# Kernel tuning notes

Measured on AMD Instinct MI355X. Metric: run time of the kernel, lower is better.

## Reference

```python
import jax, jax.numpy as jnp
import numpy as np
from jax import lax

VOCAB, EMB, H, L, B = 32000, 512, 512, 256, 64


def _flip_bwd(t):
    # t: (L, B, 2, ...); reverse time for the backward direction (dir index 1)
    return jnp.stack([t[:, :, 0], t[::-1, :, 1]], axis=2)


def sru_layer(x, W, bias, k, n_out):
    """Bidirectional SRU layer.
    x: (L, B, n_in); W: (n_in, 2*n_out*k); bias: (2, 2, n_out) = (gate{f,r}, dir, n_out).
    k=4: 4th projection is the highway input; k=3: highway uses x itself (n_in == 2*n_out).
    """
    Lx, Bx, _ = x.shape
    u = (x @ W).reshape(Lx, Bx, 2, n_out, k)
    u = _flip_bwd(u)  # both directions now scan forward in time
    f = jax.nn.sigmoid(u[..., 1] + bias[0][None, None])  # (L,B,2,n_out)
    r = jax.nn.sigmoid(u[..., 2] + bias[1][None, None])
    x_tilde = u[..., 0]

    def step(c, inp):
        f_t, xt = inp
        c = f_t * c + (1.0 - f_t) * xt
        return c, c

    c0 = jnp.zeros((Bx, 2, n_out), x.dtype)
    c_last, cs = lax.scan(step, c0, (f, x_tilde))

    if k == 4:
        x_res = u[..., 3]
    else:
        x_res = _flip_bwd(x.reshape(Lx, Bx, 2, n_out))
    h = r * jnp.tanh(cs) + (1.0 - r) * x_res
    h = _flip_bwd(h)  # restore true time order for backward dir
    return h.reshape(Lx, Bx, 2 * n_out), c_last.reshape(Bx, 2 * n_out)


def setup_inputs() -> dict:
    key = jax.random.key(0)
    ks = jax.random.split(key, 8)
    inp = {
        'padded_encoder_inputs': jax.random.randint(ks[0], (L, B), 0, VOCAB),
        'emb': jax.random.normal(ks[1], (VOCAB, EMB), jnp.float32) * 0.1,
        'W0': jax.random.normal(ks[2], (EMB, 2 * H * 4), jnp.float32) * 0.05,
        'b0': jax.random.normal(ks[3], (2, 2, H), jnp.float32) * 0.05,
        'W1': jax.random.normal(ks[4], (2 * H, 2 * H * 3), jnp.float32) * 0.05,
        'b1': jax.random.normal(ks[5], (2, 2, H), jnp.float32) * 0.05,
        'Wd': jax.random.normal(ks[6], (H, 2 * H), jnp.float32) * 0.05,
        'bd': jax.random.normal(ks[7], (H,), jnp.float32) * 0.05,
    }
    return inp


def reference(padded_encoder_inputs, emb, W0, b0, W1, b1, Wd, bd):
    # embedding lookup (dropout layers are identity in eval mode)
    x = emb[padded_encoder_inputs]            # (L, B, EMB)
    h1, c1 = sru_layer(x, W0, b0, 4, H)       # (L,B,2H), (B,2H)
    h2, c2 = sru_layer(h1, W1, b1, 3, H)
    hidden = jnp.stack([c1, c2], axis=0)      # (layers, B, 2H)
    hidden = hidden @ Wd.T + bd               # dense_hidden: (layers, B, H)
    return h2, hidden
```

## Files before the change

kernel.cpp:

```cpp
#include <hip/hip_runtime.h>

typedef __attribute__((ext_vector_type(8))) short bf16x8;
typedef __attribute__((ext_vector_type(4))) float f32x4;

__device__ __forceinline__ float b2f(ushort s) { return __uint_as_float(((uint)s) << 16); }
__device__ __forceinline__ ushort f2b(float f) {
  uint u = __float_as_uint(f);
  u += 0x7fff + ((u >> 16) & 1);
  return (ushort)(u >> 16);
}

__device__ __forceinline__ void store_h(float* p, float v) { *p = v; }
__device__ __forceinline__ void store_h(ushort* p, float v) { *p = f2b(v); }

__device__ __forceinline__ float sigm_fast(float x) { return 1.f / (1.f + __expf(-x)); }
__device__ __forceinline__ float tanh_fast(float c) {
  float e = __expf(-2.f * fabsf(c));
  float t = (1.f - e) / (1.f + e);
  return copysignf(t, c);
}

__global__ void transpose_kernel(const float* __restrict__ in, ushort* __restrict__ out,
                                 int R, int C) {
  __shared__ ushort tile[32][33];
  int bc = blockIdx.x << 5;
  int br = blockIdx.y << 5;
  int tx = threadIdx.x & 31;
  int ty = threadIdx.x >> 5;
#pragma unroll
  for (int i = 0; i < 32; i += 8)
    tile[ty + i][tx] = f2b(in[(size_t)(br + ty + i) * C + bc + tx]);
  __syncthreads();
#pragma unroll
  for (int i = 0; i < 32; i += 8)
    out[(size_t)(bc + ty + i) * R + br + tx] = tile[tx][ty + i];
}

__global__ void embed_kernel(const int* __restrict__ tok, const float* __restrict__ emb,
                             ushort* __restrict__ x) {
  int tid = threadIdx.x;
  int r = (blockIdx.x << 2) + (tid >> 6);
  int c = (tid & 63) << 3;
  int t = tok[r];
  const float* src = emb + ((size_t)t << 9) + c;
  float4 a = *(const float4*)src;
  float4 b = *(const float4*)(src + 4);
  uint4 o;
  o.x = (uint)f2b(a.x) | ((uint)f2b(a.y) << 16);
  o.y = (uint)f2b(a.z) | ((uint)f2b(a.w) << 16);
  o.z = (uint)f2b(b.x) | ((uint)f2b(b.y) << 16);
  o.w = (uint)f2b(b.z) | ((uint)f2b(b.w) << 16);
  *(uint4*)(x + ((size_t)r << 9) + c) = o;
}

__global__ __launch_bounds__(512) void gemm_bt2_kernel(
    const ushort* __restrict__ A, const ushort* __restrict__ BT,
    ushort* __restrict__ C, int M, int N, int K) {
  __shared__ ushort lds[3][24576];
  const int tid = threadIdx.x;
  const int lane = tid & 63;
  const int wave = tid >> 6;
  const int wr = wave >> 2;
  const int wc = wave & 3;

  const int xcd = blockIdx.x & 7;
  const int l = blockIdx.x >> 3;
  const int s = xcd * (gridDim.x >> 8) + (l >> 5);
  const int u = l & 31;
  const int mt = ((s & 7) << 3) + (u & 7);
  const int nt = ((s >> 3) << 2) + (u >> 3);
  const int m0 = mt << 8;
  const int n0 = nt << 7;
  const int NT = K >> 6;

  auto stage = [&](int t, int p) {
    const ushort* Asrc = A + (size_t)m0 * K + (t << 6);
    const ushort* Bsrc = BT + (size_t)n0 * K + (t << 6);
    char* base = (char*)lds[p];
#pragma unroll
    for (int i = 0; i < 6; ++i) {
      int sub = (i < 4) ? i : (i - 4);
      int off = (sub << 13) + (tid << 4);
      int row = off >> 7;
      int col = ((off & 127) ^ ((row & 7) << 4)) >> 1;
      const ushort* src = ((i < 4) ? Asrc : Bsrc) + (size_t)row * K + col;
      char* dst = base + ((i < 4) ? 0 : 32768) + (sub << 13) + (wave << 10);
      __builtin_amdgcn_global_load_lds(
          (const __attribute__((address_space(1))) void*)src,
          (__attribute__((address_space(3))) void*)dst, 16, 0, 0);
    }
  };

  f32x4 acc[8][2];
#pragma unroll
  for (int i = 0; i < 8; ++i) {
    acc[i][0] = (f32x4){0.f, 0.f, 0.f, 0.f};
    acc[i][1] = (f32x4){0.f, 0.f, 0.f, 0.f};
  }

  stage(0, 0);
  stage(1, 1);
  for (int t = 0; t < NT; ++t) {
    int p = t % 3;
    if (t + 1 < NT) {
      asm volatile("s_waitcnt vmcnt(6)" ::: "memory");
    } else {
      asm volatile("s_waitcnt vmcnt(0)" ::: "memory");
    }
    __builtin_amdgcn_s_barrier();
    __builtin_amdgcn_sched_barrier(0);
    if (t + 2 < NT) stage(t + 2, (t + 2) % 3);
    __builtin_amdgcn_sched_barrier(0);
    const char* base = (const char*)lds[p];
#pragma unroll
    for (int kk = 0; kk < 2; ++kk) {
      const int kof2 = ((kk << 5) + ((lane >> 4) << 3)) << 1;
      bf16x8 af[8], bg[2];
#pragma unroll
      for (int mi = 0; mi < 8; ++mi) {
        int row = (wr << 7) + (mi << 4) + (lane & 15);
        int byte = (row << 7) + kof2;
        byte ^= (row & 7) << 4;
        af[mi] = *(const bf16x8*)(base + byte);
      }
#pragma unroll
      for (int ni = 0; ni < 2; ++ni) {
        int row = (wc << 5) + (ni << 4) + (lane & 15);
        int byte = (row << 7) + kof2;
        byte ^= (row & 7) << 4;
        bg[ni] = *(const bf16x8*)(base + 32768 + byte);
      }
      __builtin_amdgcn_s_setprio(1);
#pragma unroll
      for (int mi = 0; mi < 8; ++mi)
#pragma unroll
        for (int ni = 0; ni < 2; ++ni)
          acc[mi][ni] =
              __builtin_amdgcn_mfma_f32_16x16x32_bf16(af[mi], bg[ni], acc[mi][ni], 0, 0, 0);
      __builtin_amdgcn_s_setprio(0);
    }
  }
#pragma unroll
  for (int mi = 0; mi < 8; ++mi) {
#pragma unroll
    for (int j = 0; j < 4; ++j) {
      int row = m0 + (wr << 7) + (mi << 4) + ((lane >> 4) << 2) + j;
      size_t bofs = (size_t)row * N + n0 + (wc << 5);
#pragma unroll
      for (int ni = 0; ni < 2; ++ni)
        C[bofs + (ni << 4) + (lane & 15)] = f2b(acc[mi][ni][j]);
    }
  }
}

template <int KC, typename OT>
__global__ void sru_scan_kernel(const ushort* __restrict__ u, const float* __restrict__ bias,
                                const ushort* __restrict__ xres, OT* __restrict__ hout,
                                float* __restrict__ cout) {
  const int L = 256, B = 64, H = 512;
  int idx = blockIdx.x * 256 + threadIdx.x;
  int h = idx & (H - 1);
  int dir = (idx >> 9) & 1;
  int b = idx >> 10;
  float bfg = bias[dir * H + h];
  float brg = bias[2 * H + dir * H + h];
  const size_t ustep = (size_t)B * 2 * H * KC;
  const ushort* ubase = u + ((size_t)b * 2 + dir) * H * KC + (size_t)h * KC;
  const size_t hstep = (size_t)B * 2 * H;
  const size_t hoff = (size_t)b * 2 * H + (size_t)dir * H + h;
  float c = 0.f;
#pragma unroll 16
  for (int s = 0; s < L; ++s) {
    int t = dir ? (L - 1 - s) : s;
    const ushort* up = ubase + (size_t)t * ustep;
    float xt, fg, rg, xr;
    if (KC == 4) {
      uint2 v = *(const uint2*)up;
      xt = b2f((ushort)(v.x & 0xffff));
      fg = b2f((ushort)(v.x >> 16));
      rg = b2f((ushort)(v.y & 0xffff));
      xr = b2f((ushort)(v.y >> 16));
    } else {
      xt = b2f(up[0]);
      fg = b2f(up[1]);
      rg = b2f(up[2]);
      xr = b2f(xres[hoff + (size_t)t * hstep]);
    }
    float f = sigm_fast(fg + bfg);
    float r = sigm_fast(rg + brg);
    c = f * c + (1.f - f) * xt;
    float hv = r * tanh_fast(c) + (1.f - r) * xr;
    store_h(hout + hoff + (size_t)t * hstep, hv);
  }
  cout[(size_t)b * 2 * H + (size_t)dir * H + h] = c;
}

__global__ __launch_bounds__(512) void dense_kernel(
    const float* __restrict__ c12, const ushort* __restrict__ WdT,
    const float* __restrict__ bd, float* __restrict__ out) {
  int row = blockIdx.x;
  int j = threadIdx.x;
  const float* c = c12 + (size_t)row * 1024;
  float acc = bd[j];
#pragma unroll 8
  for (int k = 0; k < 1024; ++k) acc += c[k] * b2f(WdT[(size_t)k * 512 + j]);
  out[(size_t)row * 512 + j] = acc;
}

extern "C" void kernel_launch(void* const* d_in, const int* in_sizes, int n_in,
                              void* d_out, int out_size, void* d_ws, size_t ws_size,
                              hipStream_t stream) {
  const int* tok = (const int*)d_in[0];
  const float* emb = (const float*)d_in[1];
  const float* W0 = (const float*)d_in[2];
  const float* b0 = (const float*)d_in[3];
  const float* W1 = (const float*)d_in[4];
  const float* b1 = (const float*)d_in[5];
  const float* Wd = (const float*)d_in[6];
  const float* bd = (const float*)d_in[7];
  float* out = (float*)d_out;

  char* ws = (char*)d_ws;
  ushort* x = (ushort*)ws;
  ushort* W0T = (ushort*)(ws + 16777216);
  ushort* W1T = (ushort*)(ws + 20971520);
  ushort* u = (ushort*)(ws + 27262976);
  ushort* h1 = (ushort*)(ws + 161480704);
  float* c12 = (float*)(ws + 195035136);
  ushort* WdT = (ushort*)(ws + 27262976 + 100663296);

  transpose_kernel<<<dim3(128, 16), 256, 0, stream>>>(W0, W0T, 512, 4096);
  transpose_kernel<<<dim3(96, 32), 256, 0, stream>>>(W1, W1T, 1024, 3072);
  embed_kernel<<<4096, 256, 0, stream>>>(tok, emb, x);
  gemm_bt2_kernel<<<2048, 512, 0, stream>>>(x, W0T, u, 16384, 4096, 512);
  sru_scan_kernel<4, ushort><<<256, 256, 0, stream>>>(u, b0, (const ushort*)nullptr, h1, c12);
  gemm_bt2_kernel<<<1536, 512, 0, stream>>>(h1, W1T, u, 16384, 3072, 1024);
  sru_scan_kernel<3, float><<<256, 256, 0, stream>>>(u, b1, h1, out, c12 + 65536);
  transpose_kernel<<<dim3(32, 16), 256, 0, stream>>>(Wd, WdT, 512, 1024);
  dense_kernel<<<128, 512, 0, stream>>>(c12, WdT, bd, out + 16777216);
}
```

Before: 407.1 us.

## Widen GEMM tile to 256x256 with double-buffered LDS pipeline

Grows the GEMM block tile along N from 128 to 256 columns, so each wave holds an 8x4 grid of MFMA accumulators and every A tile is reused twice as much. The LDS pipeline drops from three stages to two 64KB buffers, with an extra barrier after each compute step, and the grid halves. This cuts global and LDS traffic per FLOP, but raises register pressure, halves the number of blocks per GEMM and leaves only one tile of prefetch lookahead. The tile-index swizzle is unchanged but now maps onto wider N tiles.

Result: faster. 371.8 us (-8.7%).

```diff
diff --git a/kernel.cpp b/kernel.cpp
--- a/kernel.cpp
+++ b/kernel.cpp
@@ -53,10 +53,10 @@
   *(uint4*)(x + ((size_t)r << 9) + c) = o;
 }
 
-__global__ __launch_bounds__(512) void gemm_bt2_kernel(
+__global__ __launch_bounds__(512) void gemm_bt3_kernel(
     const ushort* __restrict__ A, const ushort* __restrict__ BT,
     ushort* __restrict__ C, int M, int N, int K) {
-  __shared__ ushort lds[3][24576];
+  __shared__ char lds[2][65536];
   const int tid = threadIdx.x;
   const int lane = tid & 63;
   const int wave = tid >> 6;
@@ -66,56 +66,51 @@
   const int xcd = blockIdx.x & 7;
   const int l = blockIdx.x >> 3;
   const int s = xcd * (gridDim.x >> 8) + (l >> 5);
-  const int u = l & 31;
-  const int mt = ((s & 7) << 3) + (u & 7);
-  const int nt = ((s >> 3) << 2) + (u >> 3);
+  const int uu = l & 31;
+  const int mt = ((s & 7) << 3) + (uu & 7);
+  const int nt = ((s >> 3) << 2) + (uu >> 3);
   const int m0 = mt << 8;
-  const int n0 = nt << 7;
+  const int n0 = nt << 8;
   const int NT = K >> 6;
 
   auto stage = [&](int t, int p) {
     const ushort* Asrc = A + (size_t)m0 * K + (t << 6);
     const ushort* Bsrc = BT + (size_t)n0 * K + (t << 6);
-    char* base = (char*)lds[p];
-#pragma unroll
-    for (int i = 0; i < 6; ++i) {
-      int sub = (i < 4) ? i : (i - 4);
+#pragma unroll
+    for (int i = 0; i < 8; ++i) {
+      int sub = i & 3;
       int off = (sub << 13) + (tid << 4);
       int row = off >> 7;
       int col = ((off & 127) ^ ((row & 7) << 4)) >> 1;
       const ushort* src = ((i < 4) ? Asrc : Bsrc) + (size_t)row * K + col;
-      char* dst = base + ((i < 4) ? 0 : 32768) + (sub << 13) + (wave << 10);
+      char* dst = lds[p] + ((i < 4) ? 0 : 32768) + (sub << 13) + (wave << 10);
       __builtin_amdgcn_global_load_lds(
           (const __attribute__((address_space(1))) void*)src,
           (__attribute__((address_space(3))) void*)dst, 16, 0, 0);
     }
   };
 
-  f32x4 acc[8][2];
-#pragma unroll
-  for (int i = 0; i < 8; ++i) {
-    acc[i][0] = (f32x4){0.f, 0.f, 0.f, 0.f};
-    acc[i][1] = (f32x4){0.f, 0.f, 0.f, 0.f};
-  }
+  f32x4 acc[8][4];
+#pragma unroll
+  for (int i = 0; i < 8; ++i)
+#pragma unroll
+    for (int j = 0; j < 4; ++j) acc[i][j] = (f32x4){0.f, 0.f, 0.f, 0.f};
 
   stage(0, 0);
-  stage(1, 1);
   for (int t = 0; t < NT; ++t) {
-    int p = t % 3;
+    int p = t & 1;
     if (t + 1 < NT) {
-      asm volatile("s_waitcnt vmcnt(6)" ::: "memory");
+      stage(t + 1, p ^ 1);
+      asm volatile("s_waitcnt vmcnt(8)" ::: "memory");
     } else {
       asm volatile("s_waitcnt vmcnt(0)" ::: "memory");
     }
     __builtin_amdgcn_s_barrier();
-    __builtin_amdgcn_sched_barrier(0);
-    if (t + 2 < NT) stage(t + 2, (t + 2) % 3);
-    __builtin_amdgcn_sched_barrier(0);
     const char* base = (const char*)lds[p];
 #pragma unroll
     for (int kk = 0; kk < 2; ++kk) {
       const int kof2 = ((kk << 5) + ((lane >> 4) << 3)) << 1;
-      bf16x8 af[8], bg[2];
+      bf16x8 af[8], bg[4];
 #pragma unroll
       for (int mi = 0; mi < 8; ++mi) {
         int row = (wr << 7) + (mi << 4) + (lane & 15);
@@ -124,8 +119,8 @@
         af[mi] = *(const bf16x8*)(base + byte);
       }
 #pragma unroll
-      for (int ni = 0; ni < 2; ++ni) {
-        int row = (wc << 5) + (ni << 4) + (lane & 15);
+      for (int ni = 0; ni < 4; ++ni) {
+        int row = (wc << 6) + (ni << 4) + (lane & 15);
         int byte = (row << 7) + kof2;
         byte ^= (row & 7) << 4;
         bg[ni] = *(const bf16x8*)(base + 32768 + byte);
@@ -134,20 +129,21 @@
 #pragma unroll
       for (int mi = 0; mi < 8; ++mi)
 #pragma unroll
-        for (int ni = 0; ni < 2; ++ni)
+        for (int ni = 0; ni < 4; ++ni)
           acc[mi][ni] =
               __builtin_amdgcn_mfma_f32_16x16x32_bf16(af[mi], bg[ni], acc[mi][ni], 0, 0, 0);
       __builtin_amdgcn_s_setprio(0);
     }
+    __builtin_amdgcn_s_barrier();
   }
 #pragma unroll
   for (int mi = 0; mi < 8; ++mi) {
 #pragma unroll
     for (int j = 0; j < 4; ++j) {
       int row = m0 + (wr << 7) + (mi << 4) + ((lane >> 4) << 2) + j;
-      size_t bofs = (size_t)row * N + n0 + (wc << 5);
-#pragma unroll
-      for (int ni = 0; ni < 2; ++ni)
+      size_t bofs = (size_t)row * N + n0 + (wc << 6);
+#pragma unroll
+      for (int ni = 0; ni < 4; ++ni)
         C[bofs + (ni << 4) + (lane & 15)] = f2b(acc[mi][ni][j]);
     }
   }
@@ -232,9 +228,9 @@
   transpose_kernel<<<dim3(128, 16), 256, 0, stream>>>(W0, W0T, 512, 4096);
   transpose_kernel<<<dim3(96, 32), 256, 0, stream>>>(W1, W1T, 1024, 3072);
   embed_kernel<<<4096, 256, 0, stream>>>(tok, emb, x);
-  gemm_bt2_kernel<<<2048, 512, 0, stream>>>(x, W0T, u, 16384, 4096, 512);
+  gemm_bt3_kernel<<<1024, 512, 0, stream>>>(x, W0T, u, 16384, 4096, 512);
   sru_scan_kernel<4, ushort><<<256, 256, 0, stream>>>(u, b0, (const ushort*)nullptr, h1, c12);
-  gemm_bt2_kernel<<<1536, 512, 0, stream>>>(h1, W1T, u, 16384, 3072, 1024);
+  gemm_bt3_kernel<<<768, 512, 0, stream>>>(h1, W1T, u, 16384, 3072, 1024);
   sru_scan_kernel<3, float><<<256, 256, 0, stream>>>(u, b1, h1, out, c12 + 65536);
   transpose_kernel<<<dim3(32, 16), 256, 0, stream>>>(Wd, WdT, 512, 1024);
   dense_kernel<<<128, 512, 0, stream>>>(c12, WdT, bd, out + 16777216);
```
